# Optimization experiments

Hardware: AMD Instinct MI355X
Metric: run time of the kernel (lower is better)

The kernel has to match this reference:

```python
import jax, jax.numpy as jnp
import numpy as np

NUM_HEADS = 16
NEG_INF = -9000000000000000.0


def setup_inputs() -> dict:
    key = jax.random.key(0)
    ks = jax.random.split(key, 4)
    B, S, D = 2, 2048, 1024
    x = jax.random.normal(ks[0], (B, S, D), dtype=jnp.float32)
    mask = jax.random.randint(ks[1], (1, 1, S, S), 0, 2, dtype=jnp.int32)
    # xavier-uniform-ish init scaled down for stability
    w_qkv = jax.random.normal(ks[2], (3 * D, D), dtype=jnp.float32) * (1.0 / np.sqrt(D))
    b_qkv = jnp.zeros((3 * D,), dtype=jnp.float32)
    w_o = jax.random.normal(ks[3], (D, D), dtype=jnp.float32) * (1.0 / np.sqrt(D))
    b_o = jnp.zeros((D,), dtype=jnp.float32)
    return {"x": x, "mask": mask, "w_qkv": w_qkv, "b_qkv": b_qkv, "w_o": w_o, "b_o": b_o}


def reference(x, mask, w_qkv, b_qkv, w_o, b_o):
    B, S, D = x.shape
    H = NUM_HEADS
    hd = D // H
    # qkv projection: torch Linear is x @ W.T + b
    qkv = x @ w_qkv.T + b_qkv                      # [B, S, 3D]
    qkv = qkv.reshape(B, S, H, 3 * hd).transpose(0, 2, 1, 3)  # [B, H, S, 3hd]
    q, k, v = jnp.split(qkv, 3, axis=-1)           # each [B, H, S, hd]
    scale = 1.0 / np.sqrt(hd).astype(np.float32)
    logits = jnp.einsum("bhqd,bhkd->bhqk", q, k) * scale  # [B, H, S, S]
    logits = jnp.where(mask == 0, NEG_INF, logits)
    attn = jax.nn.softmax(logits, axis=-1)
    ctx = jnp.einsum("bhqk,bhkd->bhqd", attn, v)   # [B, H, S, hd]
    ctx = ctx.transpose(0, 2, 1, 3).reshape(B, S, D)
    return ctx @ w_o.T + b_o
```

## Files before the change

### kernel.cpp

```cpp
#include <hip/hip_runtime.h>

typedef __attribute__((ext_vector_type(8))) short short8;
typedef __attribute__((ext_vector_type(4))) float f32x4;

#define MFMA16(a, b, c) __builtin_amdgcn_mfma_f32_16x16x32_bf16(a, b, c, 0, 0, 0)

#define BATCH 2
#define SEQ 2048
#define DMODEL 1024
#define NHEADS 16
#define HDIM 64
#define MROWS (BATCH * SEQ)
#define N_QKV (3 * DMODEL)

#define QSCALE 0.1803368801111184f

#define GLDS16(gp, lp)                                                       \
  __builtin_amdgcn_global_load_lds(                                          \
      (const __attribute__((address_space(1))) void*)(gp),                   \
      (__attribute__((address_space(3))) void*)(lp), 16, 0, 0)

static __device__ __forceinline__ unsigned short f2bf(float f) {
  unsigned int u = __float_as_uint(f);
  u = (u + 0x7fff + ((u >> 16) & 1)) >> 16;
  return (unsigned short)u;
}

static __device__ __forceinline__ unsigned int pk2bf(float lo, float hi) {
  unsigned int r;
  asm("v_cvt_pk_bf16_f32 %0, %1, %2" : "=v"(r) : "v"(lo), "v"(hi));
  return r;
}

__global__ void cvt_kernel(const float* __restrict__ in,
                           unsigned short* __restrict__ out, int n4) {
  int i = blockIdx.x * blockDim.x + threadIdx.x;
  if (i >= n4) return;
  f32x4 v = ((const f32x4*)in)[i];
  ushort4 o;
  o.x = f2bf(v[0]); o.y = f2bf(v[1]); o.z = f2bf(v[2]); o.w = f2bf(v[3]);
  ((ushort4*)out)[i] = o;
}

__global__ void mask_to_bits(const int* __restrict__ mask,
                             unsigned int* __restrict__ bits) {
  int i = blockIdx.x * blockDim.x + threadIdx.x;
  const int* p = mask + (size_t)i * 32;
  unsigned int v = 0;
#pragma unroll
  for (int b = 0; b < 32; ++b) v |= (p[b] != 0 ? 1u : 0u) << b;
  bits[i] = v;
}

template <int EPI>
__global__ __launch_bounds__(256) void gemm_bt(
    const unsigned short* __restrict__ A, const unsigned short* __restrict__ Bm,
    const float* __restrict__ bias, int Kdim, int Ndim,
    unsigned short* __restrict__ qb, unsigned short* __restrict__ kb,
    unsigned short* __restrict__ vtb, float* __restrict__ Cout) {
  __shared__ __align__(16) unsigned short lA[128 * 40];
  __shared__ __align__(16) unsigned short lB[128 * 40];

  int t = threadIdx.x;
  int m0 = blockIdx.y * 128, n0 = blockIdx.x * 128;
  int w = t >> 6, lane = t & 63, quad = lane >> 4, l16 = lane & 15;
  int wm = (w >> 1) * 64, wn = (w & 1) * 64;

  f32x4 acc[4][4];
#pragma unroll
  for (int i = 0; i < 4; ++i)
#pragma unroll
    for (int j = 0; j < 4; ++j) acc[i][j] = (f32x4){0.f, 0.f, 0.f, 0.f};

  int nK = Kdim >> 5;
  for (int kk = 0; kk < nK; ++kk) {
    __syncthreads();
#pragma unroll
    for (int c = 0; c < 2; ++c) {
      int id = t + c * 256;
      int row = id >> 2, c8 = (id & 3) << 3;
      *(uint4*)&lA[row * 40 + c8] =
          *(const uint4*)&A[(size_t)(m0 + row) * Kdim + (kk << 5) + c8];
      *(uint4*)&lB[row * 40 + c8] =
          *(const uint4*)&Bm[(size_t)(n0 + row) * Kdim + (kk << 5) + c8];
    }
    __syncthreads();
    short8 af[4], bfr[4];
#pragma unroll
    for (int i = 0; i < 4; ++i)
      af[i] = *(const short8*)&lA[(wm + i * 16 + l16) * 40 + quad * 8];
#pragma unroll
    for (int j = 0; j < 4; ++j)
      bfr[j] = *(const short8*)&lB[(wn + j * 16 + l16) * 40 + quad * 8];
#pragma unroll
    for (int i = 0; i < 4; ++i)
#pragma unroll
      for (int j = 0; j < 4; ++j) acc[i][j] = MFMA16(af[i], bfr[j], acc[i][j]);
  }

#pragma unroll
  for (int j = 0; j < 4; ++j) {
    int n = n0 + wn + j * 16 + l16;
    float bs = bias[n];
#pragma unroll
    for (int i = 0; i < 4; ++i) {
#pragma unroll
      for (int r = 0; r < 4; ++r) {
        int m = m0 + wm + i * 16 + quad * 4 + r;
        float v = acc[i][j][r] + bs;
        if (EPI == 0) {
          int b = m >> 11, s = m & 2047;
          int h = n / 192, rr = n % 192;
          int bh = (b << 4) + h;
          if (rr < 64)
            qb[((size_t)bh * SEQ + s) * HDIM + rr] = f2bf(v * QSCALE);
          else if (rr < 128)
            kb[((size_t)bh * SEQ + s) * HDIM + (rr - 64)] = f2bf(v);
          else
            vtb[((size_t)bh * HDIM + (rr - 128)) * SEQ + s] = f2bf(v);
        } else {
          Cout[(size_t)m * Ndim + n] = v;
        }
      }
    }
  }
}

__global__ __launch_bounds__(256, 4) void attn_kernel(
    const unsigned short* __restrict__ qbuf, const unsigned short* __restrict__ kbuf,
    const unsigned short* __restrict__ vtbuf, const unsigned int* __restrict__ mbits,
    unsigned short* __restrict__ ctx) {
  __shared__ __align__(16) unsigned short lK[2][64 * 64];
  __shared__ __align__(16) unsigned short lV[2][64 * 64];
  __shared__ __align__(16) unsigned short lP[64 * 64];

  int lin = blockIdx.y * gridDim.x + blockIdx.x;
  int slin = (lin & 7) * 128 + (lin >> 3);
  int qt = slin & 31, bh = slin >> 5;
  int q0 = qt * 64;
  const unsigned short* Q = qbuf + (size_t)bh * SEQ * HDIM;
  const unsigned short* K = kbuf + (size_t)bh * SEQ * HDIM;
  const unsigned short* VT = vtbuf + (size_t)bh * HDIM * SEQ;

  int t = threadIdx.x;
  int w = t >> 6, lane = t & 63, quad = lane >> 4, l16 = lane & 15;
  int swz = (l16 & 7) << 4;

  int qrow = q0 + w * 16 + l16;
  short8 qf0 = *(const short8*)&Q[(size_t)qrow * HDIM + quad * 8];
  short8 qf1 = *(const short8*)&Q[(size_t)qrow * HDIM + 32 + quad * 8];

  f32x4 o[4];
#pragma unroll
  for (int jt = 0; jt < 4; ++jt) o[jt] = (f32x4){0.f, 0.f, 0.f, 0.f};
  float mi = 0.f, li = 0.f;

  int scol = ((lane & 7) ^ (lane >> 3)) << 3;
  const unsigned short* gK = K + (size_t)(w * 8 + (lane >> 3)) * HDIM + scol;
  const unsigned short* gV = VT + (size_t)(w * 8 + (lane >> 3)) * SEQ + scol;

#define STAGE_KV(buf)                                            \
  do {                                                           \
    GLDS16(gK, &lK[buf][(w * 8) * 64]);                          \
    GLDS16(gK + 32 * HDIM, &lK[buf][(32 + w * 8) * 64]);         \
    GLDS16(gV, &lV[buf][(w * 8) * 64]);                          \
    GLDS16(gV + 32 * SEQ, &lV[buf][(32 + w * 8) * 64]);          \
  } while (0)

  STAGE_KV(0);
  gK += 64 * HDIM;
  gV += 64;

  const unsigned int* mrow = mbits + (size_t)qrow * 64;
  unsigned short* lPr = &lP[(w * 16 + l16) * 64];

  for (int it = 0; it < SEQ / 64; ++it) {
    __syncthreads();
    if (it + 1 < SEQ / 64) {
      STAGE_KV((it + 1) & 1);
      gK += 64 * HDIM;
      gV += 64;
    }
    const unsigned short* cK = lK[it & 1];
    const unsigned short* cV = lV[it & 1];

    uint2 mw = *(const uint2*)&mrow[it * 2];

    f32x4 s[4];
    __builtin_amdgcn_s_setprio(1);
#pragma unroll
    for (int j = 0; j < 4; ++j) {
      const char* kr = (const char*)&cK[(j * 16 + l16) * 64];
      short8 ka = *(const short8*)(kr + ((quad * 16) ^ swz));
      short8 kc = *(const short8*)(kr + ((64 + quad * 16) ^ swz));
      f32x4 z = (f32x4){0.f, 0.f, 0.f, 0.f};
      z = MFMA16(ka, qf0, z);
      z = MFMA16(kc, qf1, z);
      s[j] = z;
    }
    __builtin_amdgcn_s_setprio(0);

    unsigned int ma = mw.x >> (quad * 4);
    unsigned int mb = mw.y >> (quad * 4);
#pragma unroll
    for (int j = 0; j < 4; ++j) {
      unsigned int sel = (j < 2) ? ma : mb;
      int sh = (j & 1) << 4;
#pragma unroll
      for (int r = 0; r < 4; ++r)
        s[j][r] = (sel & (1u << (sh + r))) ? s[j][r] : -1e30f;
    }

    float x0 = fmaxf(fmaxf(s[0][0], s[0][1]), fmaxf(s[0][2], s[0][3]));
    float x1 = fmaxf(fmaxf(s[1][0], s[1][1]), fmaxf(s[1][2], s[1][3]));
    float x2 = fmaxf(fmaxf(s[2][0], s[2][1]), fmaxf(s[2][2], s[2][3]));
    float x3 = fmaxf(fmaxf(s[3][0], s[3][1]), fmaxf(s[3][2], s[3][3]));
    float mx = fmaxf(fmaxf(x0, x1), fmaxf(x2, x3));
    mx = fmaxf(mx, __shfl_xor(mx, 16));
    mx = fmaxf(mx, __shfl_xor(mx, 32));

#pragma unroll
    for (int j = 0; j < 4; ++j)
#pragma unroll
      for (int r = 0; r < 4; ++r) s[j][r] = exp2f(s[j][r] - mi);
    float r0 = (s[0][0] + s[0][1]) + (s[0][2] + s[0][3]);
    float r1 = (s[1][0] + s[1][1]) + (s[1][2] + s[1][3]);
    float r2 = (s[2][0] + s[2][1]) + (s[2][2] + s[2][3]);
    float r3 = (s[3][0] + s[3][1]) + (s[3][2] + s[3][3]);
    float rs = (r0 + r1) + (r2 + r3);

    if (!__all(mx <= mi + 5.f)) {
      float mn = fmaxf(mi, mx);
      float al = exp2f(mi - mn);
#pragma unroll
      for (int j = 0; j < 4; ++j)
#pragma unroll
        for (int r = 0; r < 4; ++r) s[j][r] *= al;
      rs *= al;
#pragma unroll
      for (int jt = 0; jt < 4; ++jt)
#pragma unroll
        for (int r = 0; r < 4; ++r) o[jt][r] *= al;
      li *= al;
      mi = mn;
    }
    rs += __shfl_xor(rs, 16);
    rs += __shfl_xor(rs, 32);
    li += rs;

#pragma unroll
    for (int j = 0; j < 4; ++j) {
      uint2 u;
      u.x = pk2bf(s[j][0], s[j][1]);
      u.y = pk2bf(s[j][2], s[j][3]);
      *(uint2*)((char*)lPr + ((j * 32 + quad * 8) ^ swz)) = u;
    }

    __builtin_amdgcn_s_setprio(1);
#pragma unroll
    for (int kh = 0; kh < 2; ++kh) {
      short8 pf = *(const short8*)((const char*)lPr + ((kh * 64 + quad * 16) ^ swz));
#pragma unroll
      for (int jt = 0; jt < 4; ++jt) {
        const char* vr = (const char*)&cV[(jt * 16 + l16) * 64];
        short8 vf = *(const short8*)(vr + ((kh * 64 + quad * 16) ^ swz));
        o[jt] = MFMA16(vf, pf, o[jt]);
      }
    }
    __builtin_amdgcn_s_setprio(0);
  }

  float inv = 1.f / li;
  int b = bh >> 4, h = bh & 15;
  unsigned short* crow = ctx + ((size_t)(b * SEQ + qrow)) * DMODEL + h * HDIM;
#pragma unroll
  for (int jt = 0; jt < 4; ++jt) {
    uint2 u;
    u.x = pk2bf(o[jt][0] * inv, o[jt][1] * inv);
    u.y = pk2bf(o[jt][2] * inv, o[jt][3] * inv);
    *(uint2*)&crow[jt * 16 + quad * 4] = u;
  }
}

extern "C" void kernel_launch(void* const* d_in, const int* in_sizes, int n_in,
                              void* d_out, int out_size, void* d_ws, size_t ws_size,
                              hipStream_t stream) {
  const float* x = (const float*)d_in[0];
  const int* mask = (const int*)d_in[1];
  const float* w_qkv = (const float*)d_in[2];
  const float* b_qkv = (const float*)d_in[3];
  const float* w_o = (const float*)d_in[4];
  const float* b_o = (const float*)d_in[5];
  float* out = (float*)d_out;

  char* ws = (char*)d_ws;
  unsigned short* xb = (unsigned short*)(ws);
  unsigned short* wqkvb = (unsigned short*)(ws + (8ull << 20));
  unsigned short* wob = (unsigned short*)(ws + (14ull << 20));
  unsigned short* qb = (unsigned short*)(ws + (16ull << 20));
  unsigned short* kb = (unsigned short*)(ws + (24ull << 20));
  unsigned short* vtb = (unsigned short*)(ws + (32ull << 20));
  unsigned short* ctx = (unsigned short*)(ws + (40ull << 20));
  unsigned int* mbits = (unsigned int*)(ws + (48ull << 20));

  cvt_kernel<<<4096, 256, 0, stream>>>(x, xb, (MROWS * DMODEL) / 4);
  cvt_kernel<<<3072, 256, 0, stream>>>(w_qkv, wqkvb, (N_QKV * DMODEL) / 4);
  cvt_kernel<<<1024, 256, 0, stream>>>(w_o, wob, (DMODEL * DMODEL) / 4);
  mask_to_bits<<<512, 256, 0, stream>>>(mask, mbits);

  gemm_bt<0><<<dim3(N_QKV / 128, MROWS / 128), 256, 0, stream>>>(
      xb, wqkvb, b_qkv, DMODEL, N_QKV, qb, kb, vtb, nullptr);

  attn_kernel<<<dim3(SEQ / 64, BATCH * NHEADS), 256, 0, stream>>>(
      qb, kb, vtb, mbits, ctx);

  gemm_bt<1><<<dim3(DMODEL / 128, MROWS / 128), 256, 0, stream>>>(
      ctx, wob, b_o, DMODEL, DMODEL, nullptr, nullptr, nullptr, out);
}
```

Baseline: 252.9 us.

## Load V from global into registers, compute row sums via MFMA, fuse conversions

Several changes at once. The attention kernel stops staging V in LDS and has each lane load its V fragments straight from global memory into registers, which frees LDS but adds uncached-pattern global loads every iteration. The softmax row sum is now accumulated with an extra MFMA against a ones vector instead of shuffle reductions, and exp2f is replaced by the raw v_exp_f32 instruction. The three fp32-to-bf16 conversion launches are merged into one kernel to save launch overhead.

```diff
diff --git a/kernel.cpp b/kernel.cpp
--- a/kernel.cpp
+++ b/kernel.cpp
@@ -32,14 +32,33 @@
   return r;
 }
 
-__global__ void cvt_kernel(const float* __restrict__ in,
-                           unsigned short* __restrict__ out, int n4) {
+static __device__ __forceinline__ float fexp2(float x) {
+  float r;
+  asm("v_exp_f32 %0, %1" : "=v"(r) : "v"(x));
+  return r;
+}
+
+__global__ void cvt3_kernel(const float* __restrict__ a, unsigned short* __restrict__ oa,
+                            int na4, const float* __restrict__ b,
+                            unsigned short* __restrict__ ob, int nb4,
+                            const float* __restrict__ c,
+                            unsigned short* __restrict__ oc, int nc4) {
   int i = blockIdx.x * blockDim.x + threadIdx.x;
-  if (i >= n4) return;
-  f32x4 v = ((const f32x4*)in)[i];
+  const float* src;
+  unsigned short* dst;
+  int j = i;
+  if (j < na4) {
+    src = a; dst = oa;
+  } else if ((j -= na4) < nb4) {
+    src = b; dst = ob;
+  } else if ((j -= nb4) < nc4) {
+    src = c; dst = oc;
+  } else
+    return;
+  f32x4 v = ((const f32x4*)src)[j];
   ushort4 o;
   o.x = f2bf(v[0]); o.y = f2bf(v[1]); o.z = f2bf(v[2]); o.w = f2bf(v[3]);
-  ((ushort4*)out)[i] = o;
+  ((ushort4*)dst)[j] = o;
 }
 
 __global__ void mask_to_bits(const int* __restrict__ mask,
@@ -131,7 +150,6 @@
     const unsigned short* __restrict__ vtbuf, const unsigned int* __restrict__ mbits,
     unsigned short* __restrict__ ctx) {
   __shared__ __align__(16) unsigned short lK[2][64 * 64];
-  __shared__ __align__(16) unsigned short lV[2][64 * 64];
   __shared__ __align__(16) unsigned short lP[64 * 64];
 
   int lin = blockIdx.y * gridDim.x + blockIdx.x;
@@ -150,26 +168,28 @@
   short8 qf0 = *(const short8*)&Q[(size_t)qrow * HDIM + quad * 8];
   short8 qf1 = *(const short8*)&Q[(size_t)qrow * HDIM + 32 + quad * 8];
 
+  const short one = (short)0x3F80;
+  short8 ones = {one, one, one, one, one, one, one, one};
+
   f32x4 o[4];
 #pragma unroll
   for (int jt = 0; jt < 4; ++jt) o[jt] = (f32x4){0.f, 0.f, 0.f, 0.f};
-  float mi = 0.f, li = 0.f;
+  f32x4 li4 = (f32x4){0.f, 0.f, 0.f, 0.f};
+  float mi = 0.f;
 
   int scol = ((lane & 7) ^ (lane >> 3)) << 3;
   const unsigned short* gK = K + (size_t)(w * 8 + (lane >> 3)) * HDIM + scol;
-  const unsigned short* gV = VT + (size_t)(w * 8 + (lane >> 3)) * SEQ + scol;
-
-#define STAGE_KV(buf)                                            \
+
+#define STAGE_K(buf)                                             \
   do {                                                           \
     GLDS16(gK, &lK[buf][(w * 8) * 64]);                          \
     GLDS16(gK + 32 * HDIM, &lK[buf][(32 + w * 8) * 64]);         \
-    GLDS16(gV, &lV[buf][(w * 8) * 64]);                          \
-    GLDS16(gV + 32 * SEQ, &lV[buf][(32 + w * 8) * 64]);          \
   } while (0)
 
-  STAGE_KV(0);
+  STAGE_K(0);
   gK += 64 * HDIM;
-  gV += 64;
+
+  const unsigned short* gV = VT + (size_t)l16 * SEQ + quad * 8;
 
   const unsigned int* mrow = mbits + (size_t)qrow * 64;
   unsigned short* lPr = &lP[(w * 16 + l16) * 64];
@@ -177,12 +197,18 @@
   for (int it = 0; it < SEQ / 64; ++it) {
     __syncthreads();
     if (it + 1 < SEQ / 64) {
-      STAGE_KV((it + 1) & 1);
+      STAGE_K((it + 1) & 1);
       gK += 64 * HDIM;
-      gV += 64;
-    }
+    }
+    short8 vf[2][4];
+#pragma unroll
+    for (int kh = 0; kh < 2; ++kh)
+#pragma unroll
+      for (int jt = 0; jt < 4; ++jt)
+        vf[kh][jt] =
+            *(const short8*)&gV[(size_t)jt * 16 * SEQ + it * 64 + kh * 32];
+
     const unsigned short* cK = lK[it & 1];
-    const unsigned short* cV = lV[it & 1];
 
     uint2 mw = *(const uint2*)&mrow[it * 2];
 
@@ -211,42 +237,37 @@
         s[j][r] = (sel & (1u << (sh + r))) ? s[j][r] : -1e30f;
     }
 
-    float x0 = fmaxf(fmaxf(s[0][0], s[0][1]), fmaxf(s[0][2], s[0][3]));
-    float x1 = fmaxf(fmaxf(s[1][0], s[1][1]), fmaxf(s[1][2], s[1][3]));
-    float x2 = fmaxf(fmaxf(s[2][0], s[2][1]), fmaxf(s[2][2], s[2][3]));
-    float x3 = fmaxf(fmaxf(s[3][0], s[3][1]), fmaxf(s[3][2], s[3][3]));
-    float mx = fmaxf(fmaxf(x0, x1), fmaxf(x2, x3));
+    float a0 = fmaxf(fmaxf(s[0][0], s[0][1]), s[0][2]);
+    float a1 = fmaxf(fmaxf(s[0][3], s[1][0]), s[1][1]);
+    float a2 = fmaxf(fmaxf(s[1][2], s[1][3]), s[2][0]);
+    float a3 = fmaxf(fmaxf(s[2][1], s[2][2]), s[2][3]);
+    float a4 = fmaxf(fmaxf(s[3][0], s[3][1]), s[3][2]);
+    float b0 = fmaxf(fmaxf(a0, a1), a2);
+    float b1 = fmaxf(fmaxf(a3, a4), s[3][3]);
+    float mx = fmaxf(b0, b1);
     mx = fmaxf(mx, __shfl_xor(mx, 16));
     mx = fmaxf(mx, __shfl_xor(mx, 32));
 
 #pragma unroll
     for (int j = 0; j < 4; ++j)
 #pragma unroll
-      for (int r = 0; r < 4; ++r) s[j][r] = exp2f(s[j][r] - mi);
-    float r0 = (s[0][0] + s[0][1]) + (s[0][2] + s[0][3]);
-    float r1 = (s[1][0] + s[1][1]) + (s[1][2] + s[1][3]);
-    float r2 = (s[2][0] + s[2][1]) + (s[2][2] + s[2][3]);
-    float r3 = (s[3][0] + s[3][1]) + (s[3][2] + s[3][3]);
-    float rs = (r0 + r1) + (r2 + r3);
+      for (int r = 0; r < 4; ++r) s[j][r] = fexp2(s[j][r] - mi);
 
     if (!__all(mx <= mi + 5.f)) {
       float mn = fmaxf(mi, mx);
-      float al = exp2f(mi - mn);
+      float al = fexp2(mi - mn);
 #pragma unroll
       for (int j = 0; j < 4; ++j)
 #pragma unroll
         for (int r = 0; r < 4; ++r) s[j][r] *= al;
-      rs *= al;
 #pragma unroll
       for (int jt = 0; jt < 4; ++jt)
 #pragma unroll
         for (int r = 0; r < 4; ++r) o[jt][r] *= al;
-      li *= al;
+#pragma unroll
+      for (int r = 0; r < 4; ++r) li4[r] *= al;
       mi = mn;
     }
-    rs += __shfl_xor(rs, 16);
-    rs += __shfl_xor(rs, 32);
-    li += rs;
 
 #pragma unroll
     for (int j = 0; j < 4; ++j) {
@@ -260,17 +281,15 @@
 #pragma unroll
     for (int kh = 0; kh < 2; ++kh) {
       short8 pf = *(const short8*)((const char*)lPr + ((kh * 64 + quad * 16) ^ swz));
-#pragma unroll
-      for (int jt = 0; jt < 4; ++jt) {
-        const char* vr = (const char*)&cV[(jt * 16 + l16) * 64];
-        short8 vf = *(const short8*)(vr + ((kh * 64 + quad * 16) ^ swz));
-        o[jt] = MFMA16(vf, pf, o[jt]);
-      }
+      li4 = MFMA16(ones, pf, li4);
+#pragma unroll
+      for (int jt = 0; jt < 4; ++jt)
+        o[jt] = MFMA16(vf[kh][jt], pf, o[jt]);
     }
     __builtin_amdgcn_s_setprio(0);
   }
 
-  float inv = 1.f / li;
+  float inv = 1.0f / li4[0];
   int b = bh >> 4, h = bh & 15;
   unsigned short* crow = ctx + ((size_t)(b * SEQ + qrow)) * DMODEL + h * HDIM;
 #pragma unroll
@@ -303,9 +322,11 @@
   unsigned short* ctx = (unsigned short*)(ws + (40ull << 20));
   unsigned int* mbits = (unsigned int*)(ws + (48ull << 20));
 
-  cvt_kernel<<<4096, 256, 0, stream>>>(x, xb, (MROWS * DMODEL) / 4);
-  cvt_kernel<<<3072, 256, 0, stream>>>(w_qkv, wqkvb, (N_QKV * DMODEL) / 4);
-  cvt_kernel<<<1024, 256, 0, stream>>>(w_o, wob, (DMODEL * DMODEL) / 4);
+  const int na4 = (MROWS * DMODEL) / 4;
+  const int nb4 = (N_QKV * DMODEL) / 4;
+  const int nc4 = (DMODEL * DMODEL) / 4;
+  cvt3_kernel<<<(na4 + nb4 + nc4 + 255) / 256, 256, 0, stream>>>(
+      x, xb, na4, w_qkv, wqkvb, nb4, w_o, wob, nc4);
   mask_to_bits<<<512, 256, 0, stream>>>(mask, mbits);
 
   gemm_bt<0><<<dim3(N_QKV / 128, MROWS / 128), 256, 0, stream>>>(
```

After: 312.1 us. 1.23x slower.
